# Kernel optimization log

Measured on AMD Instinct MI355X. Metric: run time of the kernel, lower is better.

## Reference

```python
import jax, jax.numpy as jnp
import numpy as np

NT, NV, ND, NM, NP = 50000, 1000, 20000, 5000, 8000
E = 100000
D, H, C = 256, 4, 64          # gnn_hidden_dim, heads, per-head channels
TS_FEAT, EMB, L = 64, 128, 2
NEG_SLOPE = 0.2

SIZES = {'ts': NT, 'vital': NV, 'diag': ND, 'med': NM, 'proc': NP}
EDGE_TYPES = [('ts', 'vital'), ('vital', 'ts'), ('ts', 'diag'), ('diag', 'ts'),
              ('ts', 'med'), ('med', 'ts'), ('ts', 'proc'), ('proc', 'ts')]
T = len(EDGE_TYPES)


def setup_inputs():
    key = jax.random.key(0)
    ks = jax.random.split(key, 32)
    def nrm(k, shape, s=0.05):
        return jax.random.normal(k, shape, dtype=jnp.float32) * s
    inp = {}
    inp['ts_x'] = nrm(ks[0], (NT, TS_FEAT), 1.0)
    inp['emb_vital'] = nrm(ks[1], (NV, EMB), 1.0)
    inp['emb_diag'] = nrm(ks[2], (ND, EMB), 1.0)
    inp['emb_med'] = nrm(ks[3], (NM, EMB), 1.0)
    inp['emb_proc'] = nrm(ks[4], (NP, EMB), 1.0)
    inp['Wp_ts'] = nrm(ks[5], (TS_FEAT, D)); inp['bp_ts'] = jnp.zeros((D,), jnp.float32)
    inp['Wp_c'] = nrm(ks[6], (4, EMB, D)); inp['bp_c'] = jnp.zeros((4, D), jnp.float32)
    inp['Wsrc'] = nrm(ks[7], (L, T, D, H * C))
    inp['Wdst'] = nrm(ks[8], (L, T, D, H * C))
    inp['asrc'] = nrm(ks[9], (L, T, H, C))
    inp['adst'] = nrm(ks[10], (L, T, H, C))
    inp['bconv'] = jnp.zeros((L, T, H * C), jnp.float32)
    inp['Wc1'] = nrm(ks[11], (D, D // 2)); inp['bc1'] = jnp.zeros((D // 2,), jnp.float32)
    inp['Wc2'] = nrm(ks[12], (D // 2, 1)); inp['bc2'] = jnp.zeros((1,), jnp.float32)
    names = ['ei_tv', 'ei_vt', 'ei_td', 'ei_dt', 'ei_tm', 'ei_mt', 'ei_tp', 'ei_pt']
    for i, ((s, d), nm) in enumerate(zip(EDGE_TYPES, names)):
        k1, k2 = jax.random.split(ks[13 + i])
        src = jax.random.randint(k1, (E,), 0, SIZES[s], dtype=jnp.int32)
        dst = jax.random.randint(k2, (E,), 0, SIZES[d], dtype=jnp.int32)
        inp[nm] = jnp.stack([src, dst])
    return inp


def gat_conv(xs, xd, Ws, Wd, a_s, a_d, b, ei, nd):
    """Bipartite PyG GATConv: add_self_loops=False, concat heads, eval (no dropout)."""
    hs = (xs @ Ws).reshape(-1, H, C)            # [Ns,H,C]
    hd = (xd @ Wd).reshape(-1, H, C)            # [Nd,H,C]
    es = jnp.sum(hs * a_s, axis=-1)             # [Ns,H]
    ed = jnp.sum(hd * a_d, axis=-1)             # [Nd,H]
    src, dst = ei[0], ei[1]
    e = jax.nn.leaky_relu(es[src] + ed[dst], NEG_SLOPE)   # [E,H]
    m = jax.ops.segment_max(e, dst, num_segments=nd)      # segment softmax over dst
    ex = jnp.exp(e - m[dst])
    den = jax.ops.segment_sum(ex, dst, num_segments=nd)
    alpha = ex / (den[dst] + 1e-16)
    msg = (alpha[:, :, None] * hs[src]).reshape(-1, H * C)  # [E,H*C]
    return jax.ops.segment_sum(msg, dst, num_segments=nd) + b


def _forward(ts_x, emb_vital, emb_diag, emb_med, emb_proc, Wp_ts, bp_ts, Wp_c, bp_c,
             Wsrc, Wdst, asrc, adst, bconv, Wc1, bc1, Wc2, bc2, edges):
    x = {'ts': ts_x @ Wp_ts + bp_ts,
         'vital': emb_vital @ Wp_c[0] + bp_c[0],
         'diag': emb_diag @ Wp_c[1] + bp_c[1],
         'med': emb_med @ Wp_c[2] + bp_c[2],
         'proc': emb_proc @ Wp_c[3] + bp_c[3]}
    for l in range(L):
        new = {k: jnp.zeros((SIZES[k], D), jnp.float32) for k in x}  # HeteroConv aggr='sum'
        for t, ((s, d), ei) in enumerate(zip(EDGE_TYPES, edges)):
            new[d] = new[d] + gat_conv(x[s], x[d], Wsrc[l, t], Wdst[l, t],
                                       asrc[l, t], adst[l, t], bconv[l, t], ei, SIZES[d])
        x = {k: jax.nn.relu(v) for k, v in new.items()}
    g = jnp.mean(x['ts'], axis=0)               # graph embedding
    h = jax.nn.relu(g @ Wc1 + bc1)
    logits = h @ Wc2 + bc2
    return jnp.squeeze(logits, -1)              # output_classes == 1 -> scalar


def reference(ts_x, emb_vital, emb_diag, emb_med, emb_proc, Wp_ts, bp_ts, Wp_c, bp_c,
              Wsrc, Wdst, asrc, adst, bconv, Wc1, bc1, Wc2, bc2,
              ei_tv, ei_vt, ei_td, ei_dt, ei_tm, ei_mt, ei_tp, ei_pt):
    edges = (ei_tv, ei_vt, ei_td, ei_dt, ei_tm, ei_mt, ei_tp, ei_pt)
    return _forward(ts_x, emb_vital, emb_diag, emb_med, emb_proc, Wp_ts, bp_ts, Wp_c, bp_c,
                    Wsrc, Wdst, asrc, adst, bconv, Wc1, bc1, Wc2, bc2, edges)
```

## Files before the change

### kernel.cpp

```cpp
#include <hip/hip_runtime.h>

#define E_N 100000
#define NTOT 84000
#define NDST 234000

typedef __attribute__((ext_vector_type(8))) short bfrag8;
typedef __attribute__((ext_vector_type(4))) float accf4;

__device__ __forceinline__ void atomAddF(float* p, float v) {
    unsafeAtomicAdd(p, v);
}

__device__ __forceinline__ float lrelu(float v) { return v >= 0.f ? v : 0.2f * v; }

__device__ __forceinline__ unsigned short f2bf(float f) {
    unsigned u = __float_as_uint(f);
    return (unsigned short)((u + 0x7FFFu + ((u >> 16) & 1u)) >> 16);
}
__device__ __forceinline__ float bf2f(unsigned short h) {
    return __uint_as_float(((unsigned)h) << 16);
}

__constant__ int c_tbase[8] = {0, 1000, 51000, 71000, 121000, 126000, 176000, 184000};

struct EI8 { const int* p[8]; };

struct BTJob { const float* W; unsigned short* hi; unsigned short* lo; int K; int kshift; };
struct BTBatch { BTJob j[17]; };

__global__ __launch_bounds__(256) void makeBT(BTBatch b)
{
    BTJob jb = b.j[blockIdx.z];
    int idx = blockIdx.x * 256 + threadIdx.x;
    if (idx >= (jb.K << 8)) return;
    int n = idx >> jb.kshift;
    int k = idx & (jb.K - 1);
    float w = jb.W[(size_t)k * 256 + n];
    unsigned short h = f2bf(w);
    jb.hi[idx] = h;
    jb.lo[idx] = f2bf(w - bf2f(h));
}

struct MJob { const float* A; const unsigned short* BThi; const unsigned short* BTlo;
              float* C; unsigned short* Cbf; const float* bias; int M; int K; int relu; };
struct MBatch { MJob j[8]; };

__global__ __launch_bounds__(256, 2) void gemm_mfma(MBatch batch)
{
    const MJob jb = batch.j[blockIdx.z];
    const int bx = blockIdx.x;
    const int rowblk = (bx >> 4) * 8 + (bx & 7);
    const int half = (bx >> 3) & 1;
    const int bm = rowblk * 128;
    if (bm >= jb.M) return;
    const int bn = half * 128;
    const int M = jb.M, K = jb.K;

    __shared__ unsigned short Ah[128 * 40];
    __shared__ unsigned short Al[128 * 40];
    __shared__ unsigned short B1[128 * 40];
    __shared__ unsigned short B2[128 * 40];

    const int tid  = threadIdx.x;
    const int wv   = tid >> 6;
    const int lane = tid & 63;
    const int qr = wv >> 1, qc = wv & 1;
    const int lm = lane & 15;
    const int lq = lane >> 4;

    accf4 acc[4][4] = {};

    for (int k0 = 0; k0 < K; k0 += 32) {
#pragma unroll
        for (int it = 0; it < 4; ++it) {
            int slot = it * 256 + tid;
            int m  = slot >> 3;
            int kq = (slot & 7) << 2;
            float4 v = make_float4(0.f, 0.f, 0.f, 0.f);
            if (bm + m < M) v = *(const float4*)(jb.A + (size_t)(bm + m) * K + k0 + kq);
            int o = m * 40 + kq;
            unsigned short h0 = f2bf(v.x), h1 = f2bf(v.y), h2 = f2bf(v.z), h3 = f2bf(v.w);
            Ah[o + 0] = h0; Ah[o + 1] = h1; Ah[o + 2] = h2; Ah[o + 3] = h3;
            Al[o + 0] = f2bf(v.x - bf2f(h0));
            Al[o + 1] = f2bf(v.y - bf2f(h1));
            Al[o + 2] = f2bf(v.z - bf2f(h2));
            Al[o + 3] = f2bf(v.w - bf2f(h3));
        }
#pragma unroll
        for (int it = 0; it < 2; ++it) {
            int slot = it * 256 + tid;
            int n  = slot >> 2;
            int kq = (slot & 3) << 3;
            size_t go = (size_t)(bn + n) * K + k0 + kq;
            *(uint4*)&B1[n * 40 + kq] = *(const uint4*)(jb.BThi + go);
            *(uint4*)&B2[n * 40 + kq] = *(const uint4*)(jb.BTlo + go);
        }
        __syncthreads();

        bfrag8 ah[4], al[4], b1[4], b2[4];
#pragma unroll
        for (int t = 0; t < 4; ++t) {
            int am  = qr * 64 + t * 16 + lm;
            int bnn = qc * 64 + t * 16 + lm;
            ah[t] = *(const bfrag8*)&Ah[am * 40 + lq * 8];
            al[t] = *(const bfrag8*)&Al[am * 40 + lq * 8];
            b1[t] = *(const bfrag8*)&B1[bnn * 40 + lq * 8];
            b2[t] = *(const bfrag8*)&B2[bnn * 40 + lq * 8];
        }
#pragma unroll
        for (int mt = 0; mt < 4; ++mt)
#pragma unroll
            for (int nt = 0; nt < 4; ++nt) {
                acc[mt][nt] = __builtin_amdgcn_mfma_f32_16x16x32_bf16(ah[mt], b1[nt], acc[mt][nt], 0, 0, 0);
                acc[mt][nt] = __builtin_amdgcn_mfma_f32_16x16x32_bf16(al[mt], b1[nt], acc[mt][nt], 0, 0, 0);
                acc[mt][nt] = __builtin_amdgcn_mfma_f32_16x16x32_bf16(ah[mt], b2[nt], acc[mt][nt], 0, 0, 0);
            }
        __syncthreads();
    }

#pragma unroll
    for (int nt = 0; nt < 4; ++nt) {
        int col = bn + qc * 64 + nt * 16 + lm;
        float bv = jb.bias ? jb.bias[col] : 0.f;
#pragma unroll
        for (int mt = 0; mt < 4; ++mt) {
            int row0 = bm + qr * 64 + mt * 16 + lq * 4;
#pragma unroll
            for (int r = 0; r < 4; ++r) {
                int row = row0 + r;
                if (row < M) {
                    float o = acc[mt][nt][r] + bv;
                    if (jb.relu) o = fmaxf(o, 0.f);
                    if (jb.C)   jb.C[(size_t)row * 256 + col] = o;
                    if (jb.Cbf) jb.Cbf[(size_t)row * 256 + col] = f2bf(o);
                }
            }
        }
    }
}

__global__ __launch_bounds__(256) void fill_weff(const float* __restrict__ Wsrc,
                                                 const float* __restrict__ Wdst,
                                                 const float* __restrict__ asrc,
                                                 const float* __restrict__ adst,
                                                 float* __restrict__ weff)
{
    int idx = blockIdx.x * 256 + threadIdx.x;
    if (idx >= 81920) return;
    int col = idx & 31;
    int k   = (idx >> 5) & 255;
    int lnt = idx >> 13;
    int nt  = lnt % 5;
    int l   = lnt / 5;
    bool is_src; int t, h;
    if (nt == 0) {
        if (col < 16) { is_src = true;  t = (col >> 2) * 2;            h = col & 3; }
        else          { is_src = false; t = ((col - 16) >> 2) * 2 + 1; h = col & 3; }
    } else {
        if (col < 4)      { is_src = true;  t = 2 * nt - 1; h = col; }
        else if (col < 8) { is_src = false; t = 2 * nt - 2; h = col - 4; }
        else { weff[idx] = 0.f; return; }
    }
    const float* W = (is_src ? Wsrc : Wdst) + ((size_t)((l * 8 + t) * 256 + k)) * 256 + h * 64;
    const float* a = (is_src ? asrc : adst) + ((size_t)((l * 8 + t) * 4 + h)) * 64;
    float val = 0.f;
    for (int c = 0; c < 64; c++) val += W[c] * a[c];
    weff[idx] = val;
}

template<int NO>
__device__ __forceinline__ void attnproj_body(const float* __restrict__ xrow,
                                              const float* __restrict__ W,
                                              float* __restrict__ out)
{
    float acc[NO];
#pragma unroll
    for (int j = 0; j < NO; j++) acc[j] = 0.f;
    for (int k = 0; k < 256; k += 4) {
        const float4 xv = *(const float4*)(xrow + k);
#pragma unroll
        for (int j = 0; j < NO; j++) {
            acc[j] += xv.x * W[(k + 0) * 32 + j] + xv.y * W[(k + 1) * 32 + j]
                    + xv.z * W[(k + 2) * 32 + j] + xv.w * W[(k + 3) * 32 + j];
        }
    }
#pragma unroll
    for (int j = 0; j < NO; j++) out[j] = acc[j];
}

__global__ __launch_bounds__(256) void attnproj(const float* __restrict__ x,
                                                const float* __restrict__ weff_l,
                                                float* __restrict__ attnT,
                                                float* __restrict__ attnC)
{
    int n = blockIdx.x * 256 + threadIdx.x;
    if (n >= NTOT) return;
    if (n < 50000) {
        attnproj_body<32>(x + (size_t)n * 256, weff_l, attnT + (size_t)n * 32);
    } else {
        int nt = (n < 51000) ? 1 : (n < 71000) ? 2 : (n < 76000) ? 3 : 4;
        attnproj_body<8>(x + (size_t)n * 256, weff_l + nt * 8192, attnC + (size_t)(n - 50000) * 8);
    }
}

__global__ __launch_bounds__(256) void count_k(EI8 ei, int* __restrict__ cnt)
{
    int g = blockIdx.x * 256 + threadIdx.x;
    if (g >= 8 * E_N) return;
    int t = g / E_N;
    int i = g - t * E_N;
    int d = ei.p[t][E_N + i];
    atomicAdd(&cnt[c_tbase[t] + d], 1);
}

__global__ __launch_bounds__(256) void scanA(const int* __restrict__ cnt,
                                             int* __restrict__ rowptr,
                                             int* __restrict__ bsum)
{
    __shared__ int sd[256];
    int b = blockIdx.x, t = threadIdx.x;
    int base = b * 1024 + t * 4;
    int v0 = 0, v1 = 0, v2 = 0, v3 = 0;
    if (base + 0 < NDST) v0 = cnt[base + 0];
    if (base + 1 < NDST) v1 = cnt[base + 1];
    if (base + 2 < NDST) v2 = cnt[base + 2];
    if (base + 3 < NDST) v3 = cnt[base + 3];
    int s = v0 + v1 + v2 + v3;
    sd[t] = s;
    __syncthreads();
    for (int off = 1; off < 256; off <<= 1) {
        int x = 0;
        if (t >= off) x = sd[t - off];
        __syncthreads();
        if (t >= off) sd[t] += x;
        __syncthreads();
    }
    int run = sd[t] - s;
    if (t == 255) bsum[b] = sd[255];
    if (base + 0 < NDST) rowptr[base + 0] = run;          run += v0;
    if (base + 1 < NDST) rowptr[base + 1] = run;          run += v1;
    if (base + 2 < NDST) rowptr[base + 2] = run;          run += v2;
    if (base + 3 < NDST) rowptr[base + 3] = run;
}

__global__ __launch_bounds__(256) void scanB(int* __restrict__ bsum, int nb)
{
    __shared__ int sd[256];
    int t = threadIdx.x;
    int v = (t < nb) ? bsum[t] : 0;
    sd[t] = v;
    __syncthreads();
    for (int off = 1; off < 256; off <<= 1) {
        int x = 0;
        if (t >= off) x = sd[t - off];
        __syncthreads();
        if (t >= off) sd[t] += x;
        __syncthreads();
    }
    if (t < nb) bsum[t] = sd[t] - v;
}

__global__ __launch_bounds__(256) void scanC(int* __restrict__ rowptr,
                                             const int* __restrict__ bsum,
                                             int* __restrict__ cursor)
{
    int b = blockIdx.x, t = threadIdx.x;
    int off = bsum[b];
    int base = b * 1024 + t * 4;
#pragma unroll
    for (int j = 0; j < 4; j++) {
        int i = base + j;
        if (i < NDST) {
            int r = rowptr[i] + off;
            rowptr[i] = r;
            cursor[i] = r;
        }
    }
    if (b == 0 && t == 0) rowptr[NDST] = 8 * E_N;
}

__global__ __launch_bounds__(256) void place_k(EI8 ei, int* __restrict__ cursor,
                                               int* __restrict__ ssrc)
{
    int g = blockIdx.x * 256 + threadIdx.x;
    if (g >= 8 * E_N) return;
    int t = g / E_N;
    int i = g - t * E_N;
    int d = ei.p[t][E_N + i];
    int s = ei.p[t][i];
    int pos = atomicAdd(&cursor[c_tbase[t] + d], 1);
    ssrc[pos] = s;
}

__global__ __launch_bounds__(256) void aggx_k(const float* __restrict__ attnT,
                                              const float* __restrict__ attnC,
                                              const unsigned short* __restrict__ xtsbf,
                                              const int* __restrict__ rowptr,
                                              const int* __restrict__ ssrc,
                                              float* __restrict__ aggx)
{
    int w = blockIdx.x * 4 + (threadIdx.x >> 6);
    int lane = threadIdx.x & 63;
    int h = lane >> 4;
    int ch = (h << 6) | ((lane & 15) << 2);
    int q, dloc;
    if (w < 1000)       { q = 0; dloc = w; }
    else if (w < 21000) { q = 1; dloc = w - 1000; }
    else if (w < 26000) { q = 2; dloc = w - 21000; }
    else                { q = 3; dloc = w - 26000; }
    const int csr4[4]  = {0, 51000, 121000, 176000};
    const int soff4[4] = {0, 4, 8, 12};
    int soff = soff4[q];
    int r0 = rowptr[csr4[q] + dloc], r1 = rowptr[csr4[q] + dloc + 1];
    float ed = attnC[(size_t)w * 8 + 4 + h];
    float den = 0.f, sx = 0.f, sy = 0.f, sz = 0.f, sw = 0.f;
    int e = r0;
    for (; e + 4 <= r1; e += 4) {
        int sA = ssrc[e], sB = ssrc[e + 1], sC = ssrc[e + 2], sD = ssrc[e + 3];
        float eA = attnT[(size_t)sA * 32 + soff + h];
        float eB = attnT[(size_t)sB * 32 + soff + h];
        float eC = attnT[(size_t)sC * 32 + soff + h];
        float eD = attnT[(size_t)sD * 32 + soff + h];
        ushort4 rA = *(const ushort4*)(xtsbf + (size_t)sA * 256 + ch);
        ushort4 rB = *(const ushort4*)(xtsbf + (size_t)sB * 256 + ch);
        ushort4 rC = *(const ushort4*)(xtsbf + (size_t)sC * 256 + ch);
        ushort4 rD = *(const ushort4*)(xtsbf + (size_t)sD * 256 + ch);
        float xA = __expf(lrelu(eA + ed));
        float xB = __expf(lrelu(eB + ed));
        float xC = __expf(lrelu(eC + ed));
        float xD = __expf(lrelu(eD + ed));
        den += (xA + xB) + (xC + xD);
        sx += xA * bf2f(rA.x) + xB * bf2f(rB.x) + xC * bf2f(rC.x) + xD * bf2f(rD.x);
        sy += xA * bf2f(rA.y) + xB * bf2f(rB.y) + xC * bf2f(rC.y) + xD * bf2f(rD.y);
        sz += xA * bf2f(rA.z) + xB * bf2f(rB.z) + xC * bf2f(rC.z) + xD * bf2f(rD.z);
        sw += xA * bf2f(rA.w) + xB * bf2f(rB.w) + xC * bf2f(rC.w) + xD * bf2f(rD.w);
    }
    for (; e < r1; e++) {
        int s = ssrc[e];
        float es = attnT[(size_t)s * 32 + soff + h];
        float ex = __expf(lrelu(es + ed));
        den += ex;
        ushort4 rv = *(const ushort4*)(xtsbf + (size_t)s * 256 + ch);
        sx += ex * bf2f(rv.x); sy += ex * bf2f(rv.y);
        sz += ex * bf2f(rv.z); sw += ex * bf2f(rv.w);
    }
    float inv = 1.f / (den + 1e-16f);
    float4 o; o.x = sx * inv; o.y = sy * inv; o.z = sz * inv; o.w = sw * inv;
    *(float4*)(aggx + (size_t)w * 256 + ch) = o;
}

__device__ __forceinline__ float4 agg_ts_core(const float* __restrict__ attnT,
                                              const float* __restrict__ attnC,
                                              const unsigned short* __restrict__ hscbf,
                                              const int* __restrict__ rowptr,
                                              const int* __restrict__ ssrc,
                                              const float* __restrict__ bconv_l,
                                              int d, int h, int ch)
{
    const int co4[4]   = {0, 1000, 21000, 26000};
    const int tb4[4]   = {1000, 71000, 126000, 184000};
    const int doff4[4] = {16, 20, 24, 28};
    const int bo4[4]   = {256, 768, 1280, 1792};
    int r0q[4], nq[4]; float edq[4];
    int mx = 0;
#pragma unroll
    for (int q = 0; q < 4; q++) {
        int a = rowptr[tb4[q] + d], b = rowptr[tb4[q] + d + 1];
        r0q[q] = a; nq[q] = b - a;
        mx = max(mx, b - a);
        edq[q] = attnT[(size_t)d * 32 + doff4[q] + h];
    }
    float den[4] = {0.f, 0.f, 0.f, 0.f};
    float sx[4] = {0.f, 0.f, 0.f, 0.f}, sy[4] = {0.f, 0.f, 0.f, 0.f};
    float sz[4] = {0.f, 0.f, 0.f, 0.f}, sw[4] = {0.f, 0.f, 0.f, 0.f};
    for (int i = 0; i < mx; i++) {
#pragma unroll
        for (int q = 0; q < 4; q++) {
            if (i < nq[q]) {
                int s = ssrc[r0q[q] + i];
                float es = attnC[(size_t)(co4[q] + s) * 8 + h];
                float ex = __expf(lrelu(es + edq[q]));
                den[q] += ex;
                ushort4 hv = *(const ushort4*)(hscbf + (size_t)(co4[q] + s) * 256 + ch);
                sx[q] += ex * bf2f(hv.x); sy[q] += ex * bf2f(hv.y);
                sz[q] += ex * bf2f(hv.z); sw[q] += ex * bf2f(hv.w);
            }
        }
    }
    float ax = 0.f, ay = 0.f, az = 0.f, aw = 0.f;
#pragma unroll
    for (int q = 0; q < 4; q++) {
        const float* b = bconv_l + bo4[q] + ch;
        float inv = 1.f / (den[q] + 1e-16f);
        ax += b[0] + sx[q] * inv; ay += b[1] + sy[q] * inv;
        az += b[2] + sz[q] * inv; aw += b[3] + sw[q] * inv;
    }
    float4 o;
    o.x = fmaxf(ax, 0.f); o.y = fmaxf(ay, 0.f);
    o.z = fmaxf(az, 0.f); o.w = fmaxf(aw, 0.f);
    return o;
}

__global__ __launch_bounds__(256) void agg_ts(const float* __restrict__ attnT,
                                              const float* __restrict__ attnC,
                                              const unsigned short* __restrict__ hscbf,
                                              const int* __restrict__ rowptr,
                                              const int* __restrict__ ssrc,
                                              const float* __restrict__ bconv_l,
                                              float* __restrict__ xout)
{
    int d = blockIdx.x * 4 + (threadIdx.x >> 6);
    int lane = threadIdx.x & 63;
    int h = lane >> 4;
    int ch = (h << 6) | ((lane & 15) << 2);
    float4 o = agg_ts_core(attnT, attnC, hscbf, rowptr, ssrc, bconv_l, d, h, ch);
    *(float4*)(xout + (size_t)d * 256 + ch) = o;
}

__global__ __launch_bounds__(256) void agg_ts_pool(const float* __restrict__ attnT,
                                                   const float* __restrict__ attnC,
                                                   const unsigned short* __restrict__ hscbf,
                                                   const int* __restrict__ rowptr,
                                                   const int* __restrict__ ssrc,
                                                   const float* __restrict__ bconv_l,
                                                   float* __restrict__ part)
{
    int d = blockIdx.x * 4 + (threadIdx.x >> 6);
    int lane = threadIdx.x & 63;
    int h = lane >> 4;
    int ch = (h << 6) | ((lane & 15) << 2);
    float4 o = agg_ts_core(attnT, attnC, hscbf, rowptr, ssrc, bconv_l, d, h, ch);
    __shared__ float4 red4[256];
    red4[threadIdx.x] = o;
    __syncthreads();
    if (threadIdx.x < 64) {
        float4 a = red4[threadIdx.x], b = red4[threadIdx.x + 64];
        float4 c = red4[threadIdx.x + 128], dd = red4[threadIdx.x + 192];
        float4 s;
        s.x = (a.x + b.x) + (c.x + dd.x);
        s.y = (a.y + b.y) + (c.y + dd.y);
        s.z = (a.z + b.z) + (c.z + dd.z);
        s.w = (a.w + b.w) + (c.w + dd.w);
        int cch = ((threadIdx.x >> 4) << 6) | ((threadIdx.x & 15) << 2);
        *(float4*)(part + (size_t)blockIdx.x * 256 + cch) = s;
    }
}

__global__ __launch_bounds__(256) void colsum_part(const float* __restrict__ part,
                                                   float* __restrict__ gsum)
{
    int c = threadIdx.x;
    float s = 0.f;
    for (int r = blockIdx.x; r < 12500; r += gridDim.x) s += part[(size_t)r * 256 + c];
    atomAddF(gsum + c, s);
}

__global__ __launch_bounds__(128) void head_k(const float* __restrict__ gsum,
                                              const float* __restrict__ Wc1,
                                              const float* __restrict__ bc1,
                                              const float* __restrict__ Wc2,
                                              const float* __restrict__ bc2,
                                              float* __restrict__ out)
{
    __shared__ float g[256];
    __shared__ float red[128];
    int t = threadIdx.x;
    g[t] = gsum[t] * (1.f / 50000.f);
    g[t + 128] = gsum[t + 128] * (1.f / 50000.f);
    __syncthreads();
    float acc = bc1[t];
    for (int k = 0; k < 256; k++) acc += g[k] * Wc1[k * 128 + t];
    red[t] = fmaxf(acc, 0.f) * Wc2[t];
    __syncthreads();
    for (int sft = 64; sft > 0; sft >>= 1) {
        if (t < sft) red[t] += red[t + sft];
        __syncthreads();
    }
    if (t == 0) out[0] = red[0] + bc2[0];
}

extern "C" void kernel_launch(void* const* d_in, const int* in_sizes, int n_in,
                              void* d_out, int out_size, void* d_ws, size_t ws_size,
                              hipStream_t stream)
{
    const float* ts_x   = (const float*)d_in[0];
    const float* emb[4] = {(const float*)d_in[1], (const float*)d_in[2],
                           (const float*)d_in[3], (const float*)d_in[4]};
    const float* Wp_ts  = (const float*)d_in[5];
    const float* bp_ts  = (const float*)d_in[6];
    const float* Wp_c   = (const float*)d_in[7];
    const float* bp_c   = (const float*)d_in[8];
    const float* Wsrc   = (const float*)d_in[9];
    const float* Wdst   = (const float*)d_in[10];
    const float* asrc   = (const float*)d_in[11];
    const float* adst   = (const float*)d_in[12];
    const float* bconv  = (const float*)d_in[13];
    const float* Wc1    = (const float*)d_in[14];
    const float* bc1    = (const float*)d_in[15];
    const float* Wc2    = (const float*)d_in[16];
    const float* bc2    = (const float*)d_in[17];
    EI8 ei;
    for (int t = 0; t < 8; t++) ei.p[t] = (const int*)d_in[18 + t];

    float* x0    = (float*)d_ws;
    float* x1    = x0    + 21504000;
    float* attnT = x1    + 21504000;
    float* attnC = attnT + 1600000;
    float* weff  = attnC + 272000;
    float* gsum  = weff  + 81920;
    int* rowptr  = (int*)(gsum + 256);
    int* bsum    = rowptr + 234004;
    int* ssrc    = bsum + 256;
    unsigned short* xtsbf = (unsigned short*)(ssrc + 800000);
    unsigned short* hscbf = xtsbf + 12800000;
    unsigned short* btp   = hscbf + 8704000;
    int* cursor  = (int*)hscbf;
    float* aggx  = x1;
    float* part  = x0;

    unsigned short* bt_ts_h = btp;
    unsigned short* bt_ts_l = bt_ts_h + 16384;
    unsigned short* bt_c_h[4], *bt_c_l[4];
    {
        unsigned short* p = bt_ts_l + 16384;
        for (int q = 0; q < 4; q++) { bt_c_h[q] = p; p += 32768; bt_c_l[q] = p; p += 32768; }
    }
    unsigned short* bt_w = bt_ts_l + 16384 + 8 * 32768;
    auto wpan_h = [&](int l, int t) { return bt_w + (size_t)((l == 0 ? t : 8 + t / 2) * 2) * 65536; };
    auto wpan_l = [&](int l, int t) { return wpan_h(l, t) + 65536; };

    hipMemsetAsync(cursor, 0, NDST * sizeof(int), stream);
    count_k<<<3125, 256, 0, stream>>>(ei, cursor);
    scanA<<<229, 256, 0, stream>>>(cursor, rowptr, bsum);
    scanB<<<1, 256, 0, stream>>>(bsum, 229);
    scanC<<<229, 256, 0, stream>>>(rowptr, bsum, cursor);
    place_k<<<3125, 256, 0, stream>>>(ei, cursor, ssrc);

    {
        BTBatch b = {};
        int zi = 0;
        b.j[zi++] = {Wp_ts, bt_ts_h, bt_ts_l, 64, 6};
        for (int q = 0; q < 4; q++)
            b.j[zi++] = {Wp_c + q * 32768, bt_c_h[q], bt_c_l[q], 128, 7};
        for (int t = 0; t < 8; t++)
            b.j[zi++] = {Wsrc + (size_t)(0 * 8 + t) * 65536, wpan_h(0, t), wpan_l(0, t), 256, 8};
        for (int t = 1; t < 8; t += 2)
            b.j[zi++] = {Wsrc + (size_t)(1 * 8 + t) * 65536, wpan_h(1, t), wpan_l(1, t), 256, 8};
        makeBT<<<dim3(256, 1, 17), 256, 0, stream>>>(b);
    }

    fill_weff<<<320, 256, 0, stream>>>(Wsrc, Wdst, asrc, adst, weff);

    static const int Nd4[4]    = {1000, 20000, 5000, 8000};
    static const int co4[4]    = {0, 1000, 21000, 26000};
    static const int dbase4[4] = {50000, 51000, 71000, 76000};
    static const int tsrc[4]   = {1, 3, 5, 7};
    static const int tdst[4]   = {0, 2, 4, 6};

    {
        MBatch b = {};
        b.j[0] = {ts_x, bt_ts_h, bt_ts_l, x0, xtsbf, bp_ts, 50000, 64, 0};
        for (int q = 0; q < 4; q++)
            b.j[1 + q] = {emb[q], bt_c_h[q], bt_c_l[q], x0 + (size_t)dbase4[q] * 256,
                          nullptr, bp_c + q * 256, Nd4[q], 128, 0};
        gemm_mfma<<<dim3(784, 1, 5), 256, 0, stream>>>(b);
    }

    attnproj<<<329, 256, 0, stream>>>(x0, weff, attnT, attnC);
    aggx_k<<<8500, 256, 0, stream>>>(attnT, attnC, xtsbf, rowptr, ssrc, aggx);
    {
        MBatch b = {};
        for (int q = 0; q < 4; q++)
            b.j[q] = {x0 + (size_t)dbase4[q] * 256, wpan_h(0, tsrc[q]), wpan_l(0, tsrc[q]),
                      nullptr, hscbf + (size_t)co4[q] * 256, nullptr, Nd4[q], 256, 0};
        for (int q = 0; q < 4; q++)
            b.j[4 + q] = {aggx + (size_t)co4[q] * 256, wpan_h(0, tdst[q]), wpan_l(0, tdst[q]),
                          x1 + (size_t)dbase4[q] * 256, nullptr, bconv + tdst[q] * 256, Nd4[q], 256, 1};
        gemm_mfma<<<dim3(320, 1, 8), 256, 0, stream>>>(b);
    }
    agg_ts<<<12500, 256, 0, stream>>>(attnT, attnC, hscbf, rowptr, ssrc, bconv, x1);

    attnproj<<<329, 256, 0, stream>>>(x1, weff + 40960, attnT, attnC);
    {
        MBatch b = {};
        for (int q = 0; q < 4; q++)
            b.j[q] = {x1 + (size_t)dbase4[q] * 256, wpan_h(1, tsrc[q]), wpan_l(1, tsrc[q]),
                      nullptr, hscbf + (size_t)co4[q] * 256, nullptr, Nd4[q], 256, 0};
        gemm_mfma<<<dim3(320, 1, 4), 256, 0, stream>>>(b);
    }
    agg_ts_pool<<<12500, 256, 0, stream>>>(attnT, attnC, hscbf, rowptr, ssrc, bconv + 2048, part);
    hipMemsetAsync(gsum, 0, 256 * sizeof(float), stream);
    colsum_part<<<256, 256, 0, stream>>>(part, gsum);

    head_k<<<1, 128, 0, stream>>>(gsum, Wc1, bc1, Wc2, bc2, (float*)d_out);
}
```

Before: 723.5 us.

## Fold input projections into attention weights and fuse layer-2 ts attention into aggregation

Precomputes the products of the input projection weights with the attention weight vectors, so layer-1 attention logits come straight from the raw ts features and embeddings. The fp32 ts projection x0 is no longer written. The layer-1 ts aggregation now computes the layer-2 attention logits for ts nodes from a shared-memory row instead of storing the full 256-wide ts output, which removes a large write and a later re-read. The cost is extra small kernels, a block-wide barrier and a serial 256-long dot product per lane inside the aggregation. Associativity changes may also shift numerics slightly.

```diff
diff --git a/kernel.cpp b/kernel.cpp
--- a/kernel.cpp
+++ b/kernel.cpp
@@ -168,6 +168,98 @@
     weff[idx] = val;
 }
 
+__global__ __launch_bounds__(256) void fillEff(const float* __restrict__ Wp_ts,
+                                               const float* __restrict__ bp_ts,
+                                               const float* __restrict__ Wp_c,
+                                               const float* __restrict__ bp_c,
+                                               const float* __restrict__ weff,
+                                               float* __restrict__ effT,
+                                               float* __restrict__ biasT,
+                                               float* __restrict__ effC,
+                                               float* __restrict__ biasC)
+{
+    int idx = blockIdx.x * 256 + threadIdx.x;
+    if (idx < 2048) {
+        int kk = idx >> 5, j = idx & 31;
+        float s = 0.f;
+        for (int k = 0; k < 256; k++) s += Wp_ts[kk * 256 + k] * weff[k * 32 + j];
+        effT[idx] = s;
+    } else if (idx < 2080) {
+        int j = idx - 2048;
+        float s = 0.f;
+        for (int k = 0; k < 256; k++) s += bp_ts[k] * weff[k * 32 + j];
+        biasT[j] = s;
+    } else if (idx < 2080 + 4 * 1032) {
+        int r = idx - 2080;
+        int q = r / 1032; r -= q * 1032;
+        const float* wq = weff + (q + 1) * 8192;
+        if (r < 1024) {
+            int kk = r >> 3, j = r & 7;
+            float s = 0.f;
+            for (int k = 0; k < 256; k++) s += Wp_c[(size_t)q * 32768 + kk * 256 + k] * wq[k * 32 + j];
+            effC[(q * 128 + kk) * 8 + j] = s;
+        } else {
+            int j = r - 1024;
+            float s = 0.f;
+            for (int k = 0; k < 256; k++) s += bp_c[q * 256 + k] * wq[k * 32 + j];
+            biasC[q * 8 + j] = s;
+        }
+    }
+}
+
+__global__ __launch_bounds__(256) void attnprojA(const float* __restrict__ ts_x,
+                                                 const float* __restrict__ effT,
+                                                 const float* __restrict__ biasT,
+                                                 float* __restrict__ attnT)
+{
+    int n = blockIdx.x * 256 + threadIdx.x;
+    if (n >= 50000) return;
+    float acc[32];
+#pragma unroll
+    for (int j = 0; j < 32; j++) acc[j] = biasT[j];
+    const float* xr = ts_x + (size_t)n * 64;
+    for (int k = 0; k < 64; k += 4) {
+        float4 xv = *(const float4*)(xr + k);
+#pragma unroll
+        for (int j = 0; j < 32; j++)
+            acc[j] += xv.x * effT[(k + 0) * 32 + j] + xv.y * effT[(k + 1) * 32 + j]
+                    + xv.z * effT[(k + 2) * 32 + j] + xv.w * effT[(k + 3) * 32 + j];
+    }
+#pragma unroll
+    for (int j = 0; j < 32; j++) attnT[(size_t)n * 32 + j] = acc[j];
+}
+
+__global__ __launch_bounds__(256) void attnprojC1(const float* __restrict__ e0,
+                                                  const float* __restrict__ e1,
+                                                  const float* __restrict__ e2,
+                                                  const float* __restrict__ e3,
+                                                  const float* __restrict__ effC,
+                                                  const float* __restrict__ biasC,
+                                                  float* __restrict__ attnC)
+{
+    int m = blockIdx.x * 256 + threadIdx.x;
+    if (m >= 34000) return;
+    int q, loc;
+    if (m < 1000)       { q = 0; loc = m; }
+    else if (m < 21000) { q = 1; loc = m - 1000; }
+    else if (m < 26000) { q = 2; loc = m - 21000; }
+    else                { q = 3; loc = m - 26000; }
+    const float* er = (q == 0 ? e0 : q == 1 ? e1 : q == 2 ? e2 : e3) + (size_t)loc * 128;
+    const float* W = effC + q * 1024;
+    float acc[8];
+#pragma unroll
+    for (int j = 0; j < 8; j++) acc[j] = biasC[q * 8 + j];
+    for (int k = 0; k < 128; k += 4) {
+        float4 xv = *(const float4*)(er + k);
+#pragma unroll
+        for (int j = 0; j < 8; j++)
+            acc[j] += xv.x * W[(k + 0) * 8 + j] + xv.y * W[(k + 1) * 8 + j]
+                    + xv.z * W[(k + 2) * 8 + j] + xv.w * W[(k + 3) * 8 + j];
+    }
+#pragma unroll
+    for (int j = 0; j < 8; j++) attnC[(size_t)m * 8 + j] = acc[j];
+}
+
 template<int NO>
 __device__ __forceinline__ void attnproj_body(const float* __restrict__ xrow,
                                               const float* __restrict__ W,
@@ -188,19 +280,15 @@
     for (int j = 0; j < NO; j++) out[j] = acc[j];
 }
 
-__global__ __launch_bounds__(256) void attnproj(const float* __restrict__ x,
-                                                const float* __restrict__ weff_l,
-                                                float* __restrict__ attnT,
-                                                float* __restrict__ attnC)
-{
-    int n = blockIdx.x * 256 + threadIdx.x;
-    if (n >= NTOT) return;
-    if (n < 50000) {
-        attnproj_body<32>(x + (size_t)n * 256, weff_l, attnT + (size_t)n * 32);
-    } else {
-        int nt = (n < 51000) ? 1 : (n < 71000) ? 2 : (n < 76000) ? 3 : 4;
-        attnproj_body<8>(x + (size_t)n * 256, weff_l + nt * 8192, attnC + (size_t)(n - 50000) * 8);
-    }
+__global__ __launch_bounds__(256) void attnprojC2(const float* __restrict__ x1,
+                                                  const float* __restrict__ weff_l,
+                                                  float* __restrict__ attnC)
+{
+    int m = blockIdx.x * 256 + threadIdx.x;
+    if (m >= 34000) return;
+    int n = 50000 + m;
+    int nt = (n < 51000) ? 1 : (n < 71000) ? 2 : (n < 76000) ? 3 : 4;
+    attnproj_body<8>(x1 + (size_t)n * 256, weff_l + nt * 8192, attnC + (size_t)m * 8);
 }
 
 __global__ __launch_bounds__(256) void count_k(EI8 ei, int* __restrict__ cnt)
@@ -401,20 +489,31 @@
     return o;
 }
 
-__global__ __launch_bounds__(256) void agg_ts(const float* __restrict__ attnT,
-                                              const float* __restrict__ attnC,
-                                              const unsigned short* __restrict__ hscbf,
-                                              const int* __restrict__ rowptr,
-                                              const int* __restrict__ ssrc,
-                                              const float* __restrict__ bconv_l,
-                                              float* __restrict__ xout)
-{
-    int d = blockIdx.x * 4 + (threadIdx.x >> 6);
+__global__ __launch_bounds__(256) void agg_ts_fold(float* __restrict__ attnT,
+                                                   const float* __restrict__ attnC,
+                                                   const unsigned short* __restrict__ hscbf,
+                                                   const int* __restrict__ rowptr,
+                                                   const int* __restrict__ ssrc,
+                                                   const float* __restrict__ bconv_l,
+                                                   const float* __restrict__ weff2)
+{
+    int wv = threadIdx.x >> 6;
+    int d = blockIdx.x * 4 + wv;
     int lane = threadIdx.x & 63;
     int h = lane >> 4;
     int ch = (h << 6) | ((lane & 15) << 2);
     float4 o = agg_ts_core(attnT, attnC, hscbf, rowptr, ssrc, bconv_l, d, h, ch);
-    *(float4*)(xout + (size_t)d * 256 + ch) = o;
+    __shared__ float rowbuf[4][256];
+    rowbuf[wv][ch + 0] = o.x; rowbuf[wv][ch + 1] = o.y;
+    rowbuf[wv][ch + 2] = o.z; rowbuf[wv][ch + 3] = o.w;
+    __syncthreads();
+    if (lane < 16) {
+        int j = 16 + lane;
+        const float* rb = rowbuf[wv];
+        float s = 0.f;
+        for (int c = 0; c < 256; c++) s += rb[c] * weff2[c * 32 + j];
+        attnT[(size_t)d * 32 + j] = s;
+    }
 }
 
 __global__ __launch_bounds__(256) void agg_ts_pool(const float* __restrict__ attnT,
@@ -508,7 +607,11 @@
     float* attnC = attnT + 1600000;
     float* weff  = attnC + 272000;
     float* gsum  = weff  + 81920;
-    int* rowptr  = (int*)(gsum + 256);
+    float* effT  = gsum  + 256;
+    float* biasT = effT  + 2048;
+    float* effC  = biasT + 32;
+    float* biasC = effC  + 4096;
+    int* rowptr  = (int*)(biasC + 32);
     int* bsum    = rowptr + 234004;
     int* ssrc    = bsum + 256;
     unsigned short* xtsbf = (unsigned short*)(ssrc + 800000);
@@ -550,6 +653,10 @@
     }
 
     fill_weff<<<320, 256, 0, stream>>>(Wsrc, Wdst, asrc, adst, weff);
+    fillEff<<<25, 256, 0, stream>>>(Wp_ts, bp_ts, Wp_c, bp_c, weff, effT, biasT, effC, biasC);
+
+    attnprojA<<<196, 256, 0, stream>>>(ts_x, effT, biasT, attnT);
+    attnprojC1<<<133, 256, 0, stream>>>(emb[0], emb[1], emb[2], emb[3], effC, biasC, attnC);
 
     static const int Nd4[4]    = {1000, 20000, 5000, 8000};
     static const int co4[4]    = {0, 1000, 21000, 26000};
@@ -559,14 +666,13 @@
 
     {
         MBatch b = {};
-        b.j[0] = {ts_x, bt_ts_h, bt_ts_l, x0, xtsbf, bp_ts, 50000, 64, 0};
+        b.j[0] = {ts_x, bt_ts_h, bt_ts_l, nullptr, xtsbf, bp_ts, 50000, 64, 0};
         for (int q = 0; q < 4; q++)
             b.j[1 + q] = {emb[q], bt_c_h[q], bt_c_l[q], x0 + (size_t)dbase4[q] * 256,
                           nullptr, bp_c + q * 256, Nd4[q], 128, 0};
         gemm_mfma<<<dim3(784, 1, 5), 256, 0, stream>>>(b);
     }
 
-    attnproj<<<329, 256, 0, stream>>>(x0, weff, attnT, attnC);
     aggx_k<<<8500, 256, 0, stream>>>(attnT, attnC, xtsbf, rowptr, ssrc, aggx);
     {
         MBatch b = {};
@@ -578,9 +684,9 @@
                           x1 + (size_t)dbase4[q] * 256, nullptr, bconv + tdst[q] * 256, Nd4[q], 256, 1};
         gemm_mfma<<<dim3(320, 1, 8), 256, 0, stream>>>(b);
     }
-    agg_ts<<<12500, 256, 0, stream>>>(attnT, attnC, hscbf, rowptr, ssrc, bconv, x1);
-
-    attnproj<<<329, 256, 0, stream>>>(x1, weff + 40960, attnT, attnC);
+    agg_ts_fold<<<12500, 256, 0, stream>>>(attnT, attnC, hscbf, rowptr, ssrc, bconv, weff + 40960);
+
+    attnprojC2<<<133, 256, 0, stream>>>(x1, weff + 40960, attnC);
     {
         MBatch b = {};
         for (int q = 0; q < 4; q++)
```

After: 746.3 us. 1.03x slower.
